# Performance work log

Hardware: AMD Instinct MI355X
Metric: run time of the kernel (lower is better)

## Reference

```python
import jax, jax.numpy as jnp
import numpy as np

LORA_ALPHA = 16.0

def setup_inputs() -> dict:
    key = jax.random.key(0)
    kx, kw, ka, kb, kbias = jax.random.split(key, 5)
    B_, S, D_in, D_out, R = 2, 4096, 4096, 4096, 16
    x = jax.random.normal(kx, (B_, S, D_in), dtype=jnp.float32)
    W = jax.random.normal(kw, (D_out, D_in), dtype=jnp.float32) * 0.02
    A = jax.random.normal(ka, (R, D_in), dtype=jnp.float32) * 0.02
    Bm = jax.random.normal(kb, (D_out, R), dtype=jnp.float32) * 0.02
    bias = jax.random.normal(kbias, (D_out,), dtype=jnp.float32) * 0.02
    return {"x": x, "W": W, "A": A, "B": Bm, "bias": bias}

def reference(x, W, A, B, bias):
    # y = x @ W.T + bias + (alpha/rank) * (x @ A.T) @ B.T   (dropout p=0)
    rank = A.shape[0]
    lora_scale = LORA_ALPHA / rank
    y = jnp.einsum('bsd,nd->bsn', x, W) + bias
    h = jnp.einsum('bsd,rd->bsr', x, A)          # [B,S,r] low-rank down-proj
    y = y + lora_scale * jnp.einsum('bsr,nr->bsn', h, B)
    return y
```

## Files before the change

### kernel.cpp

```cpp
#include <hip/hip_runtime.h>
#include <hip/hip_bf16.h>

typedef short bf16x8 __attribute__((ext_vector_type(8)));
typedef float f32x4 __attribute__((ext_vector_type(4)));
typedef unsigned short ushort8v __attribute__((ext_vector_type(8)));

#define VMWAIT(n) asm volatile("s_waitcnt vmcnt(" #n ")" ::: "memory")
#define SBAR() asm volatile("s_barrier" ::: "memory")

__device__ __forceinline__ unsigned short f2bf(float f) {
  unsigned u = __builtin_bit_cast(unsigned, f);
  u += 0x7fffu + ((u >> 16) & 1u);
  return (unsigned short)(u >> 16);
}

__device__ __forceinline__ void gload_lds16(const unsigned short* g, unsigned short* l) {
  __builtin_amdgcn_global_load_lds((const __attribute__((address_space(1))) void*)g,
                                   (__attribute__((address_space(3))) void*)l, 16, 0, 0);
}

__global__ __launch_bounds__(256) void cast_x_kernel(const float* __restrict__ in,
                                                     unsigned short* __restrict__ out,
                                                     int n8) {
  int i = blockIdx.x * 256 + threadIdx.x;
  if (i >= n8) return;
  const float4* p = (const float4*)in + (size_t)i * 2;
  float4 a = p[0], b = p[1];
  ushort8v v;
  v[0] = f2bf(a.x); v[1] = f2bf(a.y); v[2] = f2bf(a.z); v[3] = f2bf(a.w);
  v[4] = f2bf(b.x); v[5] = f2bf(b.y); v[6] = f2bf(b.z); v[7] = f2bf(b.w);
  *((ushort8v*)out + i) = v;
}

__global__ __launch_bounds__(256) void make_weff_kernel(const float* __restrict__ W,
                                                        const float* __restrict__ A,
                                                        const float* __restrict__ Bm,
                                                        unsigned short* __restrict__ out,
                                                        float scale, int K, int R, int total8) {
  int idx = blockIdx.x * 256 + threadIdx.x;
  if (idx >= total8) return;
  int perRow = K >> 3;
  int n = idx / perRow;
  int d0 = (idx - n * perRow) << 3;
  const float4* wp = (const float4*)(W + (size_t)n * K + d0);
  float4 w0 = wp[0], w1 = wp[1];
  float acc[8] = {w0.x, w0.y, w0.z, w0.w, w1.x, w1.y, w1.z, w1.w};
#pragma unroll 4
  for (int r = 0; r < R; ++r) {
    float c = Bm[(size_t)n * R + r] * scale;
    const float4* ap = (const float4*)(A + (size_t)r * K + d0);
    float4 a0 = ap[0], a1 = ap[1];
    acc[0] += c * a0.x; acc[1] += c * a0.y; acc[2] += c * a0.z; acc[3] += c * a0.w;
    acc[4] += c * a1.x; acc[5] += c * a1.y; acc[6] += c * a1.z; acc[7] += c * a1.w;
  }
  ushort8v v;
#pragma unroll
  for (int j = 0; j < 8; ++j) v[j] = f2bf(acc[j]);
  *((ushort8v*)out + idx) = v;
}

__global__ __launch_bounds__(512, 2) void gemm256_bt_bias(const unsigned short* __restrict__ Xb,
                                                          const unsigned short* __restrict__ Wb,
                                                          const float* __restrict__ bias,
                                                          float* __restrict__ C,
                                                          int M, int N, int K) {
  __shared__ __align__(16) unsigned short lds[4][16384];
  const int t = threadIdx.x;
  const int wave = t >> 6, lane = t & 63;
  const int fr = lane & 15, kc = lane >> 4;
  const int wr = wave >> 2, wc = wave & 3;

  const int NTn = N >> 8;
  const int nwg = gridDim.x;
  int bid = blockIdx.x;
  if ((nwg & 7) == 0) bid = (bid & 7) * (nwg >> 3) + (bid >> 3);
  const int tm = bid / NTn, tn = bid % NTn;
  const int m0 = tm << 8, n0 = tn << 8;

  const int srow = t >> 2;
  const int gch  = (t & 3) ^ ((t >> 3) & 3);
  const unsigned short* gA0 = Xb + (size_t)(m0 + srow) * K + gch * 8;
  const unsigned short* gA1 = gA0 + (size_t)128 * K;
  const unsigned short* gB0 = Wb + (size_t)(n0 + srow) * K + gch * 8;
  const unsigned short* gB1 = gB0 + (size_t)128 * K;
  const int stA0 = wave * 512;
  const int stA1 = 4096 + wave * 512;
  const int stB0 = 8192 + wave * 512;
  const int stB1 = 12288 + wave * 512;

  int offA[8], offB[4];
#pragma unroll
  for (int m = 0; m < 8; ++m) {
    int row = wr * 128 + m * 16 + fr;
    offA[m] = row * 64 + (((kc ^ (row >> 1)) & 3) << 4);
  }
#pragma unroll
  for (int n = 0; n < 4; ++n) {
    int row = wc * 64 + n * 16 + fr;
    offB[n] = 16384 + row * 64 + (((kc ^ (row >> 1)) & 3) << 4);
  }

  f32x4 acc[8][4];
#pragma unroll
  for (int m = 0; m < 8; ++m)
#pragma unroll
    for (int n = 0; n < 4; ++n) acc[m][n] = (f32x4){0.f, 0.f, 0.f, 0.f};

  const int NT = K >> 5;

#define STAGE(tt) do {                                   \
    unsigned short* sb_ = &lds[(tt) & 3][0];             \
    const int ko_ = (tt) * 32;                           \
    gload_lds16(gA0 + ko_, sb_ + stA0);                  \
    gload_lds16(gA1 + ko_, sb_ + stA1);                  \
    gload_lds16(gB0 + ko_, sb_ + stB0);                  \
    gload_lds16(gB1 + ko_, sb_ + stB1);                  \
  } while (0)

#define COMPUTE(tt) do {                                                          \
    const char* p_ = (const char*)&lds[(tt) & 3][0];                              \
    bf16x8 av_[4], bv_[4];                                                        \
    _Pragma("unroll") for (int n = 0; n < 4; ++n)                                 \
      bv_[n] = *(const bf16x8*)(p_ + offB[n]);                                    \
    _Pragma("unroll") for (int m = 0; m < 4; ++m)                                 \
      av_[m] = *(const bf16x8*)(p_ + offA[m]);                                    \
    __builtin_amdgcn_s_setprio(1);                                                \
    _Pragma("unroll") for (int m = 0; m < 4; ++m)                                 \
      _Pragma("unroll") for (int n = 0; n < 4; ++n)                               \
        acc[m][n] = __builtin_amdgcn_mfma_f32_16x16x32_bf16(av_[m], bv_[n], acc[m][n], 0, 0, 0); \
    __builtin_amdgcn_s_setprio(0);                                                \
    _Pragma("unroll") for (int m = 0; m < 4; ++m)                                 \
      av_[m] = *(const bf16x8*)(p_ + offA[4 + m]);                                \
    __builtin_amdgcn_s_setprio(1);                                                \
    _Pragma("unroll") for (int m = 0; m < 4; ++m)                                 \
      _Pragma("unroll") for (int n = 0; n < 4; ++n)                               \
        acc[4 + m][n] = __builtin_amdgcn_mfma_f32_16x16x32_bf16(av_[m], bv_[n], acc[4 + m][n], 0, 0, 0); \
    __builtin_amdgcn_s_setprio(0);                                                \
  } while (0)

  STAGE(0); STAGE(1); STAGE(2);
  int tt = 0;
  for (; tt < NT - 3; ++tt) {
    STAGE(tt + 3);
    VMWAIT(12);
    SBAR();
    COMPUTE(tt);
    SBAR();
  }
  VMWAIT(8);  SBAR(); COMPUTE(NT - 3); SBAR();
  VMWAIT(4);  SBAR(); COMPUTE(NT - 2); SBAR();
  VMWAIT(0);  SBAR(); COMPUTE(NT - 1);

  const int crow = (lane >> 4) * 4;
  const int ccol = lane & 15;
#pragma unroll
  for (int n = 0; n < 4; ++n) {
    int col = n0 + wc * 64 + n * 16 + ccol;
    float bv = bias[col];
#pragma unroll
    for (int m = 0; m < 8; ++m) {
      int row = m0 + wr * 128 + m * 16 + crow;
      float* cp = C + (size_t)row * N + col;
#pragma unroll
      for (int r = 0; r < 4; ++r) cp[(size_t)r * N] = acc[m][n][r] + bv;
    }
  }
#undef STAGE
#undef COMPUTE
}

__global__ __launch_bounds__(256) void gemm_bt_bias(const unsigned short* __restrict__ Xb,
                                                    const unsigned short* __restrict__ Wb,
                                                    const float* __restrict__ bias,
                                                    float* __restrict__ C,
                                                    int M, int N, int K) {
  __shared__ unsigned short sA[128 * 32];
  __shared__ unsigned short sB[128 * 32];
  const int t = threadIdx.x;
  const int wave = t >> 6, lane = t & 63;
  const int NT = N >> 7;
  const int nwg = gridDim.x;
  int bid = blockIdx.x;
  if ((nwg & 7) == 0) bid = (bid & 7) * (nwg >> 3) + (bid >> 3);
  const int tm = bid / NT, tn = bid % NT;
  const int m0 = tm << 7, n0 = tn << 7;
  const int wr = wave >> 1, wc = wave & 1;

  f32x4 acc[4][4];
#pragma unroll
  for (int m = 0; m < 4; ++m)
#pragma unroll
    for (int n = 0; n < 4; ++n) acc[m][n] = (f32x4){0.f, 0.f, 0.f, 0.f};

  const unsigned short* gA0 = Xb + (size_t)(m0 + (t >> 2)) * K + (t & 3) * 8;
  const unsigned short* gA1 = Xb + (size_t)(m0 + 64 + (t >> 2)) * K + (t & 3) * 8;
  const unsigned short* gB0 = Wb + (size_t)(n0 + (t >> 2)) * K + (t & 3) * 8;
  const unsigned short* gB1 = Wb + (size_t)(n0 + 64 + (t >> 2)) * K + (t & 3) * 8;
  unsigned short* lA0 = sA + (size_t)(wave * 64) * 8;
  unsigned short* lA1 = sA + (size_t)(256 + wave * 64) * 8;
  unsigned short* lB0 = sB + (size_t)(wave * 64) * 8;
  unsigned short* lB1 = sB + (size_t)(256 + wave * 64) * 8;

  const int rrow = lane & 15;
  const int rk = (lane >> 4) * 8;

  for (int k0 = 0; k0 < K; k0 += 32) {
    gload_lds16(gA0 + k0, lA0);
    gload_lds16(gA1 + k0, lA1);
    gload_lds16(gB0 + k0, lB0);
    gload_lds16(gB1 + k0, lB1);
    __syncthreads();
    bf16x8 af[4], bfr[4];
#pragma unroll
    for (int m = 0; m < 4; ++m)
      af[m] = *(const bf16x8*)&sA[(size_t)(wr * 64 + m * 16 + rrow) * 32 + rk];
#pragma unroll
    for (int n = 0; n < 4; ++n)
      bfr[n] = *(const bf16x8*)&sB[(size_t)(wc * 64 + n * 16 + rrow) * 32 + rk];
#pragma unroll
    for (int m = 0; m < 4; ++m)
#pragma unroll
      for (int n = 0; n < 4; ++n)
        acc[m][n] = __builtin_amdgcn_mfma_f32_16x16x32_bf16(af[m], bfr[n], acc[m][n], 0, 0, 0);
    __syncthreads();
  }
  const int crow0 = (lane >> 4) * 4;
  const int ccol = lane & 15;
#pragma unroll
  for (int n = 0; n < 4; ++n) {
    int col = n0 + wc * 64 + n * 16 + ccol;
    float bv = bias[col];
#pragma unroll
    for (int m = 0; m < 4; ++m) {
      int row = m0 + wr * 64 + m * 16 + crow0;
      float* cp = C + (size_t)row * N + col;
#pragma unroll
      for (int r = 0; r < 4; ++r) cp[(size_t)r * N] = acc[m][n][r] + bv;
    }
  }
}

__global__ __launch_bounds__(64) void lora_h_kernel(const float* __restrict__ x,
                                                    const float* __restrict__ A,
                                                    float* __restrict__ h,
                                                    float scale, int K, int R) {
  int m = blockIdx.x, lane = threadIdx.x;
  float acc[16];
#pragma unroll
  for (int r = 0; r < 16; ++r) acc[r] = 0.f;
  for (int d = lane; d < K; d += 64) {
    float xv = x[(size_t)m * K + d];
    for (int r = 0; r < R; ++r) acc[r] += xv * A[(size_t)r * K + d];
  }
  for (int off = 32; off; off >>= 1)
    for (int r = 0; r < R; ++r) acc[r] += __shfl_down(acc[r], off);
  if (lane == 0)
    for (int r = 0; r < R; ++r) h[(size_t)m * R + r] = acc[r] * scale;
}

__global__ __launch_bounds__(256) void fgemm_fallback(const float* __restrict__ X,
                                                      const float* __restrict__ W,
                                                      const float* __restrict__ Bm,
                                                      const float* __restrict__ bias,
                                                      const float* __restrict__ h,
                                                      float* __restrict__ C,
                                                      int M, int N, int K, int R) {
  __shared__ float sX[64][20];
  __shared__ float sW[64][20];
  int nt = N >> 6;
  int bx = blockIdx.x % nt, by = blockIdx.x / nt;
  int m0 = by << 6, n0 = bx << 6;
  int t = threadIdx.x;
  int tx = t & 15, ty = t >> 4;
  float acc[4][4] = {};
  int lr = t >> 2, lc = (t & 3) << 2;
  for (int k0 = 0; k0 < K; k0 += 16) {
    *(float4*)&sX[lr][lc] = *(const float4*)&X[(size_t)(m0 + lr) * K + k0 + lc];
    *(float4*)&sW[lr][lc] = *(const float4*)&W[(size_t)(n0 + lr) * K + k0 + lc];
    __syncthreads();
#pragma unroll
    for (int kk = 0; kk < 16; ++kk) {
      float a[4], b[4];
#pragma unroll
      for (int i = 0; i < 4; ++i) a[i] = sX[ty * 4 + i][kk];
#pragma unroll
      for (int j = 0; j < 4; ++j) b[j] = sW[tx * 4 + j][kk];
#pragma unroll
      for (int i = 0; i < 4; ++i)
#pragma unroll
        for (int j = 0; j < 4; ++j) acc[i][j] += a[i] * b[j];
    }
    __syncthreads();
  }
#pragma unroll
  for (int i = 0; i < 4; ++i) {
    int row = m0 + ty * 4 + i;
#pragma unroll
    for (int j = 0; j < 4; ++j) {
      int col = n0 + tx * 4 + j;
      float lo = 0.f;
      for (int r = 0; r < R; ++r) lo += h[(size_t)row * R + r] * Bm[(size_t)col * R + r];
      C[(size_t)row * N + col] = acc[i][j] + bias[col] + lo;
    }
  }
}

extern "C" void kernel_launch(void* const* d_in, const int* in_sizes, int n_in,
                              void* d_out, int out_size, void* d_ws, size_t ws_size,
                              hipStream_t stream) {
  const float* x    = (const float*)d_in[0];
  const float* W    = (const float*)d_in[1];
  const float* A    = (const float*)d_in[2];
  const float* Bm   = (const float*)d_in[3];
  const float* bias = (const float*)d_in[4];
  float* out = (float*)d_out;

  const int N = in_sizes[4];
  const int R = in_sizes[3] / N;
  const int K = in_sizes[2] / R;
  const int M = in_sizes[0] / K;
  const float scale = 16.0f / (float)R;

  const size_t xbytes = (size_t)M * K * 2;
  const size_t wbytes = (size_t)N * K * 2;
  const bool ws_ok = (ws_size >= xbytes + wbytes);
  const bool fast256 = ws_ok && (M % 256 == 0) && (N % 256 == 0) && (K % 32 == 0) && (K >= 128);
  const bool fast128 = ws_ok && (M % 128 == 0) && (N % 128 == 0) && (K % 32 == 0);

  if (fast256 || fast128) {
    unsigned short* xb = (unsigned short*)d_ws;
    unsigned short* wb = (unsigned short*)((char*)d_ws + xbytes);
    int n8 = M * K / 8;
    cast_x_kernel<<<dim3((n8 + 255) / 256), dim3(256), 0, stream>>>(x, xb, n8);
    int t8 = N * K / 8;
    make_weff_kernel<<<dim3((t8 + 255) / 256), dim3(256), 0, stream>>>(W, A, Bm, wb, scale, K, R, t8);
    if (fast256) {
      int grid = (M / 256) * (N / 256);
      gemm256_bt_bias<<<dim3(grid), dim3(512), 0, stream>>>(xb, wb, bias, out, M, N, K);
    } else {
      int grid = (M / 128) * (N / 128);
      gemm_bt_bias<<<dim3(grid), dim3(256), 0, stream>>>(xb, wb, bias, out, M, N, K);
    }
  } else {
    float* h = (float*)d_ws;
    lora_h_kernel<<<dim3(M), dim3(64), 0, stream>>>(x, A, h, scale, K, R);
    int grid = (M / 64) * (N / 64);
    fgemm_fallback<<<dim3(grid), dim3(256), 0, stream>>>(x, W, Bm, bias, h, out, M, N, K, R);
  }
}
```

Before: 358.6 us.

## Interleave global-to-LDS staging with MFMA halves and fuse prep kernels

Splits the per-tile global-to-LDS loads into A and B halves and issues them between the two MFMA half-blocks, with explicit lgkmcnt waits, sched barriers and extra s_barriers so load issue overlaps compute. The vmcnt wait is moved after the second half's staging. The x cast and the effective-weight build are merged into one launch to cut a kernel launch. It adds more barriers per tile, which could cost throughput if the interleaving doesn't hide latency.

```diff
diff --git a/kernel.cpp b/kernel.cpp
--- a/kernel.cpp
+++ b/kernel.cpp
@@ -5,8 +5,9 @@
 typedef float f32x4 __attribute__((ext_vector_type(4)));
 typedef unsigned short ushort8v __attribute__((ext_vector_type(8)));
 
-#define VMWAIT(n) asm volatile("s_waitcnt vmcnt(" #n ")" ::: "memory")
 #define SBAR() asm volatile("s_barrier" ::: "memory")
+#define LGKM0() do { asm volatile("s_waitcnt lgkmcnt(0)" ::: "memory"); \
+    __builtin_amdgcn_sched_barrier(0); } while (0)
 
 __device__ __forceinline__ unsigned short f2bf(float f) {
   unsigned u = __builtin_bit_cast(unsigned, f);
@@ -19,26 +20,25 @@
                                    (__attribute__((address_space(3))) void*)l, 16, 0, 0);
 }
 
-__global__ __launch_bounds__(256) void cast_x_kernel(const float* __restrict__ in,
-                                                     unsigned short* __restrict__ out,
-                                                     int n8) {
+__global__ __launch_bounds__(256) void prep_kernel(const float* __restrict__ x,
+                                                   const float* __restrict__ W,
+                                                   const float* __restrict__ A,
+                                                   const float* __restrict__ Bm,
+                                                   unsigned short* __restrict__ xb,
+                                                   unsigned short* __restrict__ wb,
+                                                   float scale, int K, int R, int n8, int t8) {
   int i = blockIdx.x * 256 + threadIdx.x;
-  if (i >= n8) return;
-  const float4* p = (const float4*)in + (size_t)i * 2;
-  float4 a = p[0], b = p[1];
-  ushort8v v;
-  v[0] = f2bf(a.x); v[1] = f2bf(a.y); v[2] = f2bf(a.z); v[3] = f2bf(a.w);
-  v[4] = f2bf(b.x); v[5] = f2bf(b.y); v[6] = f2bf(b.z); v[7] = f2bf(b.w);
-  *((ushort8v*)out + i) = v;
-}
-
-__global__ __launch_bounds__(256) void make_weff_kernel(const float* __restrict__ W,
-                                                        const float* __restrict__ A,
-                                                        const float* __restrict__ Bm,
-                                                        unsigned short* __restrict__ out,
-                                                        float scale, int K, int R, int total8) {
-  int idx = blockIdx.x * 256 + threadIdx.x;
-  if (idx >= total8) return;
+  if (i < n8) {
+    const float4* p = (const float4*)x + (size_t)i * 2;
+    float4 a = p[0], b = p[1];
+    ushort8v v;
+    v[0] = f2bf(a.x); v[1] = f2bf(a.y); v[2] = f2bf(a.z); v[3] = f2bf(a.w);
+    v[4] = f2bf(b.x); v[5] = f2bf(b.y); v[6] = f2bf(b.z); v[7] = f2bf(b.w);
+    *((ushort8v*)xb + i) = v;
+    return;
+  }
+  int idx = i - n8;
+  if (idx >= t8) return;
   int perRow = K >> 3;
   int n = idx / perRow;
   int d0 = (idx - n * perRow) << 3;
@@ -56,7 +56,7 @@
   ushort8v v;
 #pragma unroll
   for (int j = 0; j < 8; ++j) v[j] = f2bf(acc[j]);
-  *((ushort8v*)out + idx) = v;
+  *((ushort8v*)wb + idx) = v;
 }
 
 __global__ __launch_bounds__(512, 2) void gemm256_bt_bias(const unsigned short* __restrict__ Xb,
@@ -108,48 +108,57 @@
 
   const int NT = K >> 5;
 
-#define STAGE(tt) do {                                   \
+#define STAGE_A(tt) do {                                 \
     unsigned short* sb_ = &lds[(tt) & 3][0];             \
     const int ko_ = (tt) * 32;                           \
     gload_lds16(gA0 + ko_, sb_ + stA0);                  \
     gload_lds16(gA1 + ko_, sb_ + stA1);                  \
+  } while (0)
+#define STAGE_B(tt) do {                                 \
+    unsigned short* sb_ = &lds[(tt) & 3][0];             \
+    const int ko_ = (tt) * 32;                           \
     gload_lds16(gB0 + ko_, sb_ + stB0);                  \
     gload_lds16(gB1 + ko_, sb_ + stB1);                  \
   } while (0)
 
-#define COMPUTE(tt) do {                                                          \
+#define TILE(tt, DOSTAGE, VM) do {                                                \
     const char* p_ = (const char*)&lds[(tt) & 3][0];                              \
     bf16x8 av_[4], bv_[4];                                                        \
     _Pragma("unroll") for (int n = 0; n < 4; ++n)                                 \
       bv_[n] = *(const bf16x8*)(p_ + offB[n]);                                    \
     _Pragma("unroll") for (int m = 0; m < 4; ++m)                                 \
       av_[m] = *(const bf16x8*)(p_ + offA[m]);                                    \
+    if (DOSTAGE) { STAGE_A((tt) + 3); }                                           \
+    SBAR();                                                                       \
+    LGKM0();                                                                      \
     __builtin_amdgcn_s_setprio(1);                                                \
     _Pragma("unroll") for (int m = 0; m < 4; ++m)                                 \
       _Pragma("unroll") for (int n = 0; n < 4; ++n)                               \
         acc[m][n] = __builtin_amdgcn_mfma_f32_16x16x32_bf16(av_[m], bv_[n], acc[m][n], 0, 0, 0); \
     __builtin_amdgcn_s_setprio(0);                                                \
+    SBAR();                                                                       \
     _Pragma("unroll") for (int m = 0; m < 4; ++m)                                 \
       av_[m] = *(const bf16x8*)(p_ + offA[4 + m]);                                \
+    if (DOSTAGE) { STAGE_B((tt) + 3); }                                           \
+    asm volatile("s_waitcnt vmcnt(" VM ")" ::: "memory");                         \
+    SBAR();                                                                       \
+    LGKM0();                                                                      \
     __builtin_amdgcn_s_setprio(1);                                                \
     _Pragma("unroll") for (int m = 0; m < 4; ++m)                                 \
       _Pragma("unroll") for (int n = 0; n < 4; ++n)                               \
         acc[4 + m][n] = __builtin_amdgcn_mfma_f32_16x16x32_bf16(av_[m], bv_[n], acc[4 + m][n], 0, 0, 0); \
     __builtin_amdgcn_s_setprio(0);                                                \
+    SBAR();                                                                       \
   } while (0)
 
-  STAGE(0); STAGE(1); STAGE(2);
-  int tt = 0;
-  for (; tt < NT - 3; ++tt) {
-    STAGE(tt + 3);
-    VMWAIT(12);
-    SBAR();
-    COMPUTE(tt);
-    SBAR();
-  }
-  VMWAIT(8);  SBAR(); COMPUTE(NT - 3); SBAR();
-  VMWAIT(4);  SBAR(); COMPUTE(NT - 2); SBAR();
-  VMWAIT(0);  SBAR(); COMPUTE(NT - 1);
+  STAGE_A(0); STAGE_B(0); STAGE_A(1); STAGE_B(1); STAGE_A(2); STAGE_B(2);
+  asm volatile("s_waitcnt vmcnt(8)" ::: "memory");
+  SBAR();
+
+  for (int tt = 0; tt < NT - 3; ++tt) TILE(tt, 1, "8");
+  TILE(NT - 3, 0, "4");
+  TILE(NT - 2, 0, "0");
+  TILE(NT - 1, 0, "0");
 
   const int crow = (lane >> 4) * 4;
   const int ccol = lane & 15;
@@ -165,8 +174,9 @@
       for (int r = 0; r < 4; ++r) cp[(size_t)r * N] = acc[m][n][r] + bv;
     }
   }
-#undef STAGE
-#undef COMPUTE
+#undef STAGE_A
+#undef STAGE_B
+#undef TILE
 }
 
 __global__ __launch_bounds__(256) void gemm_bt_bias(const unsigned short* __restrict__ Xb,
@@ -331,9 +341,10 @@
     unsigned short* xb = (unsigned short*)d_ws;
     unsigned short* wb = (unsigned short*)((char*)d_ws + xbytes);
     int n8 = M * K / 8;
-    cast_x_kernel<<<dim3((n8 + 255) / 256), dim3(256), 0, stream>>>(x, xb, n8);
     int t8 = N * K / 8;
-    make_weff_kernel<<<dim3((t8 + 255) / 256), dim3(256), 0, stream>>>(W, A, Bm, wb, scale, K, R, t8);
+    int total = n8 + t8;
+    prep_kernel<<<dim3((total + 255) / 256), dim3(256), 0, stream>>>(x, W, A, Bm, xb, wb,
+                                                                     scale, K, R, n8, t8);
     if (fast256) {
       int grid = (M / 256) * (N / 256);
       gemm256_bt_bias<<<dim3(grid), dim3(512), 0, stream>>>(xb, wb, bias, out, M, N, K);
```

New measurement: 346.1 us. -3.5%, faster.
